# Kernel optimization log

Measured on AMD Instinct MI355X. Metric: run time of the kernel, lower is better.

Reference implementation:

```python
import math
import jax, jax.numpy as jnp
import numpy as np

B, T, D, DFF, E, K = 2, 4096, 1024, 2048, 8, 2
CAP_FACTOR = 1.25


def setup_inputs() -> dict:
    key = jax.random.key(0)
    ks = jax.random.split(key, 5)
    x = jax.random.normal(ks[0], (B, T, D), dtype=jnp.float32)
    gate_w = jax.random.normal(ks[1], (E, D), dtype=jnp.float32) * 0.02
    W1 = jax.random.normal(ks[2], (E, D, DFF), dtype=jnp.float32) * 0.02
    b1 = jnp.zeros((E, DFF), dtype=jnp.float32)
    W2 = jax.random.normal(ks[3], (E, DFF, D), dtype=jnp.float32) * 0.02
    b2 = jnp.zeros((E, D), dtype=jnp.float32)
    return {"x": x, "gate_w": gate_w, "W1": W1, "b1": b1, "W2": W2, "b2": b2}


def _moe_forward(x, gate_w, W1, b1, W2, b2):
    Bs, Ts, Ds = x.shape
    N = Bs * Ts
    x_flat = x.reshape(N, Ds)

    # --- router ---
    logits = x_flat @ gate_w.T                          # (N, E)
    probs = jax.nn.softmax(logits, axis=-1)             # (N, E)
    top_w, top_i = jax.lax.top_k(probs, K)              # (N, K)
    disp_w = top_w / (jnp.sum(top_w, axis=-1, keepdims=True) + 1e-9)

    # --- capacity: slot-major, token-order priority (matches the Python loops) ---
    capacity = max(1, int(math.ceil(CAP_FACTOR * N * K / E)))
    idx_flat = top_i.T.reshape(-1)                       # (K*N,) slot-major order
    oh = jax.nn.one_hot(idx_flat, E, dtype=jnp.int32)    # (K*N, E)
    # position of each assignment within its expert's arrival order
    pos = jnp.sum(jnp.cumsum(oh, axis=0) * oh, axis=-1) - 1  # (K*N,)
    keep = (pos < capacity).reshape(K, N).T              # (N, K)
    w_capped = disp_w * keep.astype(disp_w.dtype)        # (N, K)

    # --- combine weights per expert ---
    oh_nke = jax.nn.one_hot(top_i, E, dtype=w_capped.dtype)   # (N, K, E)
    comb = jnp.einsum('nk,nke->ne', w_capped, oh_nke)         # (N, E)

    # --- experts: dense per-expert FFN, zero-weight tokens contribute nothing ---
    out = jnp.zeros_like(x_flat)
    for e in range(E):
        h = jax.nn.gelu(x_flat @ W1[e] + b1[e], approximate=False)  # (N, DFF)
        y = h @ W2[e] + b2[e]                                        # (N, D)
        out = out + comb[:, e:e + 1] * y

    # --- Switch-style aux load-balancing loss ---
    assigned = (jnp.sum(oh_nke, axis=1) > 0).astype(probs.dtype)  # (N, E)
    f = jnp.mean(assigned, axis=0)
    p = jnp.mean(probs, axis=0)
    aux_loss = E * jnp.sum(f * p)

    return out.reshape(Bs, Ts, Ds), aux_loss


def reference(x, gate_w, W1, b1, W2, b2):
    return _moe_forward(x, gate_w, W1, b1, W2, b2)
```

## Files before the change

kernel.cpp:

```cpp
#include <hip/hip_runtime.h>
#include <hip/hip_bf16.h>
#include <math.h>

#define NB   2
#define NT   4096
#define ND   1024
#define NDFF 2048
#define NE   8
#define NK   2
#define NN   (NB * NT)
#define NCAP 2560

typedef unsigned short ushort_t;
typedef __attribute__((ext_vector_type(8))) short bf16x8;
typedef __attribute__((ext_vector_type(8))) unsigned short u16x8;
typedef __attribute__((ext_vector_type(4))) float f32x4;

__device__ __forceinline__ float gelu_exact(float v) {
  return 0.5f * v * (1.0f + erff(v * 0.70710678118654752f));
}

__device__ __forceinline__ unsigned short f2bf(float f) {
  unsigned int u = __float_as_uint(f);
  u += 0x7fffu + ((u >> 16) & 1u);
  return (unsigned short)(u >> 16);
}
__device__ __forceinline__ float bf2f(unsigned short h) {
  return __uint_as_float(((unsigned int)h) << 16);
}

__device__ __forceinline__ void gl_lds16(const void* g, void* l) {
  __builtin_amdgcn_global_load_lds(
      (__attribute__((address_space(1))) void*)g,
      (__attribute__((address_space(3))) void*)l, 16, 0, 0);
}

__global__ __launch_bounds__(256) void router_kernel(
    const float* __restrict__ x, const float* __restrict__ gw,
    int* __restrict__ top_i, float* __restrict__ disp_w,
    float* __restrict__ p_sum, int* __restrict__ f_cnt) {
  __shared__ float s_p[NE];
  __shared__ int s_f[NE];
  if (threadIdx.x < NE) { s_p[threadIdx.x] = 0.0f; s_f[threadIdx.x] = 0; }
  __syncthreads();

  const int lane = threadIdx.x & 63;
  const int wv = threadIdx.x >> 6;
  const int n = blockIdx.x * 4 + wv;

  const float4* xr = (const float4*)(x + (size_t)n * ND);
  float acc[NE];
#pragma unroll
  for (int e = 0; e < NE; ++e) acc[e] = 0.0f;

#pragma unroll
  for (int q = 0; q < 4; ++q) {
    float4 xv = xr[lane * 4 + q];
#pragma unroll
    for (int e = 0; e < NE; ++e) {
      float4 g = ((const float4*)(gw + (size_t)e * ND))[lane * 4 + q];
      acc[e] += xv.x * g.x + xv.y * g.y + xv.z * g.z + xv.w * g.w;
    }
  }
#pragma unroll
  for (int m = 1; m < 64; m <<= 1) {
#pragma unroll
    for (int e = 0; e < NE; ++e) acc[e] += __shfl_xor(acc[e], m, 64);
  }

  float mx = acc[0];
#pragma unroll
  for (int e = 1; e < NE; ++e) mx = fmaxf(mx, acc[e]);
  float p[NE];
  float s = 0.0f;
#pragma unroll
  for (int e = 0; e < NE; ++e) { p[e] = expf(acc[e] - mx); s += p[e]; }
  float inv = 1.0f / s;
#pragma unroll
  for (int e = 0; e < NE; ++e) p[e] *= inv;

  int i1 = 0; float v1 = p[0];
#pragma unroll
  for (int e = 1; e < NE; ++e) { if (p[e] > v1) { v1 = p[e]; i1 = e; } }
  int i2 = 0; float v2 = -1.0f;
#pragma unroll
  for (int e = 0; e < NE; ++e) { if (e != i1 && p[e] > v2) { v2 = p[e]; i2 = e; } }

  if (lane == 0) {
    float dsum = v1 + v2 + 1e-9f;
    top_i[n * NK + 0] = i1;
    top_i[n * NK + 1] = i2;
    disp_w[n * NK + 0] = v1 / dsum;
    disp_w[n * NK + 1] = v2 / dsum;
#pragma unroll
    for (int e = 0; e < NE; ++e) atomicAdd(&s_p[e], p[e]);
    atomicAdd(&s_f[i1], 1);
    atomicAdd(&s_f[i2], 1);
  }
  __syncthreads();
  if (threadIdx.x < NE) {
    atomicAdd(&p_sum[threadIdx.x], s_p[threadIdx.x]);
    atomicAdd(&f_cnt[threadIdx.x], s_f[threadIdx.x]);
  }
}

__global__ __launch_bounds__(512) void scan_kernel(
    const int* __restrict__ top_i, const float* __restrict__ disp_w,
    int* __restrict__ routed_tok, float* __restrict__ routed_w,
    int* __restrict__ counts, const float* __restrict__ p_sum,
    const int* __restrict__ f_cnt, float* __restrict__ aux_out) {
  __shared__ __align__(16) int s_top[NN * NK];
  for (int i = threadIdx.x; i < (NN * NK) / 4; i += 512)
    ((int4*)s_top)[i] = ((const int4*)top_i)[i];
  __syncthreads();

  const int e = threadIdx.x >> 6;
  const int lane = threadIdx.x & 63;
  int cnt = 0;
  for (int c = 0; c < (NN * NK) / 64; ++c) {
    int a = c * 64 + lane;
    int n = a & (NN - 1);
    int k = a >> 13;
    bool m = (s_top[n * NK + k] == e);
    unsigned long long mask = __ballot(m);
    if (m) {
      int pos = cnt + __popcll(mask & ((1ull << lane) - 1ull));
      if (pos < NCAP) {
        routed_tok[e * NCAP + pos] = n;
        routed_w[e * NCAP + pos] = disp_w[n * NK + k];
      }
    }
    cnt += (int)__popcll(mask);
  }
  if (lane == 0) counts[e] = (cnt < NCAP) ? cnt : NCAP;

  if (threadIdx.x == 0) {
    float aux = 0.0f;
    for (int j = 0; j < NE; ++j)
      aux += (p_sum[j] / (float)NN) * ((float)f_cnt[j] / (float)NN);
    aux_out[0] = aux * (float)NE;
  }
}

__global__ __launch_bounds__(256) void tsplit_kernel(
    const float* __restrict__ W, ushort_t* __restrict__ Thi,
    ushort_t* __restrict__ Tlo, int K, int N) {
  __shared__ float tile[32][33];
  const int t = threadIdx.x;
  const int n0 = blockIdx.x * 32, k0 = blockIdx.y * 32;
  const int r = t >> 3, c4 = (t & 7) * 4;
  float4 v = *(const float4*)(W + (size_t)blockIdx.z * K * N +
                              (size_t)(k0 + r) * N + n0 + c4);
  tile[r][c4 + 0] = v.x; tile[r][c4 + 1] = v.y;
  tile[r][c4 + 2] = v.z; tile[r][c4 + 3] = v.w;
  __syncthreads();
  const int n = t >> 3, kc = (t & 7) * 4;
  ushort4 h, l;
  float f;
  f = tile[kc + 0][n]; h.x = f2bf(f); l.x = f2bf(f - bf2f(h.x));
  f = tile[kc + 1][n]; h.y = f2bf(f); l.y = f2bf(f - bf2f(h.y));
  f = tile[kc + 2][n]; h.z = f2bf(f); l.z = f2bf(f - bf2f(h.z));
  f = tile[kc + 3][n]; h.w = f2bf(f); l.w = f2bf(f - bf2f(h.w));
  size_t o = (size_t)blockIdx.z * N * K + (size_t)(n0 + n) * K + k0 + kc;
  *(ushort4*)(Thi + o) = h;
  *(ushort4*)(Tlo + o) = l;
}

__global__ __launch_bounds__(512, 2) void fgemm_fused(
    const float* __restrict__ x,
    const ushort_t* __restrict__ w1hi, const ushort_t* __restrict__ w1lo,
    const float* __restrict__ b1,
    const ushort_t* __restrict__ w2hi, const ushort_t* __restrict__ w2lo,
    const float* __restrict__ b2,
    const ushort_t* __restrict__ Hrhi, const ushort_t* __restrict__ Hrlo,
    ushort_t* __restrict__ Hwhi, ushort_t* __restrict__ Hwlo,
    const int* __restrict__ routed_tok, const float* __restrict__ routed_w,
    const int* __restrict__ counts, float* __restrict__ outf,
    int n_g1_z, int g1_lo, int g2_lo, int Rh) {
  const int bz = blockIdx.z;
  const bool isG1 = bz < n_g1_z;
  const int e = isG1 ? bz : bz - n_g1_z;
  const int count = counts[e];
  const int chunk_lo = isG1 ? g1_lo : g2_lo;
  const int local0 = blockIdx.y * 128;
  const int row0 = chunk_lo + local0;
  if (row0 >= count) return;
  const int bx = blockIdx.x;
  const int col0 = isG1 ? bx * 256 : (bx & 3) * 256;
  const int koff = isG1 ? 0 : (bx >> 2) * 1024;
  const int Ntot = isG1 ? NDFF : ND;
  const int Bstride = isG1 ? ND : NDFF;

  __shared__ __align__(16) char lds[49152];
  char* ldsA = lds;
  char* ldsB = lds + 16384;

  const int t = threadIdx.x;
  const int lane = t & 63;
  const int wid = t >> 6;
  const int wr = wid >> 2, wc = wid & 3;
  const int fr = lane & 15, ko = lane >> 4;

  const float* srcAf = nullptr;
  char* dstH_ = nullptr; char* dstL_ = nullptr;
  const ushort_t* srcA[2];
  if (isG1) {
    const int r = t >> 2, kc = t & 3;
    const int rr = row0 + r;
    const int tok = routed_tok[e * NCAP + (rr < count ? rr : 0)];
    srcAf = x + (size_t)tok * ND + kc * 8;
    dstH_ = ldsA + (size_t)(r * 8 + (kc ^ (r & 7))) * 16;
    dstL_ = ldsA + (size_t)(r * 8 + ((kc + 4) ^ (r & 7))) * 16;
  } else {
#pragma unroll
    for (int c = 0; c < 2; ++c) {
      int ci = t + 512 * c;
      int r = ci >> 3, bp = ci & 7;
      int bs = bp ^ (r & 7);
      size_t arow = (size_t)e * Rh + local0 + r;
      srcA[c] = (bs < 4 ? Hrhi : Hrlo) + arow * (size_t)NDFF + koff + (bs & 3) * 8;
    }
  }
  const ushort_t* Bh = isG1 ? w1hi : w2hi;
  const ushort_t* Bl = isG1 ? w1lo : w2lo;
  const ushort_t* srcB[4];
#pragma unroll
  for (int c = 0; c < 4; ++c) {
    int ci = t + 512 * c;
    int cc = ci >> 3, bp = ci & 7;
    int bs = bp ^ (cc & 7);
    srcB[c] = (bs < 4 ? Bh : Bl) +
              ((size_t)e * Ntot + col0 + cc) * (size_t)Bstride + koff + (bs & 3) * 8;
  }

  f32x4 acc[4][4] = {};

  for (int ks = 0; ks < 1024; ks += 32) {
    if (isG1) {
      float4 v0 = *(const float4*)(srcAf);
      float4 v1 = *(const float4*)(srcAf + 4);
      srcAf += 32;
      u16x8 hh, ll;
      unsigned short h; float f;
      f = v0.x; h = f2bf(f); hh[0] = h; ll[0] = f2bf(f - bf2f(h));
      f = v0.y; h = f2bf(f); hh[1] = h; ll[1] = f2bf(f - bf2f(h));
      f = v0.z; h = f2bf(f); hh[2] = h; ll[2] = f2bf(f - bf2f(h));
      f = v0.w; h = f2bf(f); hh[3] = h; ll[3] = f2bf(f - bf2f(h));
      f = v1.x; h = f2bf(f); hh[4] = h; ll[4] = f2bf(f - bf2f(h));
      f = v1.y; h = f2bf(f); hh[5] = h; ll[5] = f2bf(f - bf2f(h));
      f = v1.z; h = f2bf(f); hh[6] = h; ll[6] = f2bf(f - bf2f(h));
      f = v1.w; h = f2bf(f); hh[7] = h; ll[7] = f2bf(f - bf2f(h));
      *(u16x8*)dstH_ = hh;
      *(u16x8*)dstL_ = ll;
    } else {
#pragma unroll
      for (int c = 0; c < 2; ++c) {
        gl_lds16(srcA[c], ldsA + (c * 512 + wid * 64) * 16);
        srcA[c] += 32;
      }
    }
#pragma unroll
    for (int c = 0; c < 4; ++c) {
      gl_lds16(srcB[c], ldsB + (c * 512 + wid * 64) * 16);
      srcB[c] += 32;
    }
    __syncthreads();

    bf16x8 Ah[4], Al[4], Bhf[4], Blf[4];
#pragma unroll
    for (int fi = 0; fi < 4; ++fi) {
      int r = wr * 64 + fi * 16 + fr;
      Ah[fi] = *(const bf16x8*)(ldsA + r * 128 + ((ko ^ (r & 7)) << 4));
      Al[fi] = *(const bf16x8*)(ldsA + r * 128 + (((4 + ko) ^ (r & 7)) << 4));
    }
#pragma unroll
    for (int fj = 0; fj < 4; ++fj) {
      int cc = wc * 64 + fj * 16 + fr;
      Bhf[fj] = *(const bf16x8*)(ldsB + cc * 128 + ((ko ^ (cc & 7)) << 4));
      Blf[fj] = *(const bf16x8*)(ldsB + cc * 128 + (((4 + ko) ^ (cc & 7)) << 4));
    }
#pragma unroll
    for (int fi = 0; fi < 4; ++fi)
#pragma unroll
      for (int fj = 0; fj < 4; ++fj) {
        acc[fi][fj] = __builtin_amdgcn_mfma_f32_16x16x32_bf16(
            Ah[fi], Bhf[fj], acc[fi][fj], 0, 0, 0);
        acc[fi][fj] = __builtin_amdgcn_mfma_f32_16x16x32_bf16(
            Ah[fi], Blf[fj], acc[fi][fj], 0, 0, 0);
        acc[fi][fj] = __builtin_amdgcn_mfma_f32_16x16x32_bf16(
            Al[fi], Bhf[fj], acc[fi][fj], 0, 0, 0);
      }
    __syncthreads();
  }

  const float* bias = isG1 ? b1 : b2;
  float bv[4];
#pragma unroll
  for (int fj = 0; fj < 4; ++fj)
    bv[fj] = (koff == 0)
                 ? bias[(size_t)e * Ntot + col0 + wc * 64 + fj * 16 + fr]
                 : 0.0f;

  if (isG1) {
#pragma unroll
    for (int fi = 0; fi < 4; ++fi) {
#pragma unroll
      for (int rg = 0; rg < 4; ++rg) {
        int rr = row0 + wr * 64 + fi * 16 + ko * 4 + rg;
        if (rr < count) {
          size_t rb = ((size_t)e * Rh + (rr - chunk_lo)) * (size_t)NDFF;
#pragma unroll
          for (int fj = 0; fj < 4; ++fj) {
            int cc = col0 + wc * 64 + fj * 16 + fr;
            float g = gelu_exact(acc[fi][fj][rg] + bv[fj]);
            unsigned short hh = f2bf(g);
            Hwhi[rb + cc] = hh;
            Hwlo[rb + cc] = f2bf(g - bf2f(hh));
          }
        }
      }
    }
  } else {
#pragma unroll
    for (int fi = 0; fi < 4; ++fi) {
#pragma unroll
      for (int rg = 0; rg < 4; ++rg) {
        int rr = row0 + wr * 64 + fi * 16 + ko * 4 + rg;
        if (rr < count) {
          int tok = routed_tok[e * NCAP + rr];
          float wgt = routed_w[e * NCAP + rr];
          float* orow = outf + (size_t)tok * ND;
#pragma unroll
          for (int fj = 0; fj < 4; ++fj) {
            int cc = col0 + wc * 64 + fj * 16 + fr;
            atomicAdd(orow + cc, wgt * (acc[fi][fj][rg] + bv[fj]));
          }
        }
      }
    }
  }
}

__global__ __launch_bounds__(256) void gemm1_kernel(
    const float* __restrict__ x, const float* __restrict__ W1,
    const float* __restrict__ b1, const int* __restrict__ routed_tok,
    const int* __restrict__ counts, float* __restrict__ H,
    int e0, size_t h_stride) {
  const int e = e0 + blockIdx.z;
  const int count = counts[e];
  const int row0 = blockIdx.y * 128;
  if (row0 >= count) return;
  const int col0 = blockIdx.x * 128;
  const float* W = W1 + (size_t)e * ND * NDFF;
  float* Hb = H + (size_t)blockIdx.z * h_stride;

  __shared__ __align__(16) float As[16][128];
  __shared__ __align__(16) float Bs[16][128];

  const int tid = threadIdx.x;
  const int arow = tid >> 1;
  const int aq = (tid & 1) * 8;
  const int r = row0 + arow;
  const int tok = routed_tok[e * NCAP + (r < count ? r : 0)];
  const float* Arow = x + (size_t)tok * ND;
  const int bk = tid >> 5;
  const int bc = (tid & 31) * 4;
  const int ty = tid >> 4, tx = tid & 15;

  float c[8][8] = {};

  for (int k0 = 0; k0 < ND; k0 += 16) {
    float4 av0 = *(const float4*)(Arow + k0 + aq);
    float4 av1 = *(const float4*)(Arow + k0 + aq + 4);
    float4 bv0 = *(const float4*)(W + (size_t)(k0 + bk) * NDFF + col0 + bc);
    float4 bv1 = *(const float4*)(W + (size_t)(k0 + bk + 8) * NDFF + col0 + bc);
    __syncthreads();
    As[aq + 0][arow] = av0.x; As[aq + 1][arow] = av0.y;
    As[aq + 2][arow] = av0.z; As[aq + 3][arow] = av0.w;
    As[aq + 4][arow] = av1.x; As[aq + 5][arow] = av1.y;
    As[aq + 6][arow] = av1.z; As[aq + 7][arow] = av1.w;
    *(float4*)&Bs[bk][bc] = bv0;
    *(float4*)&Bs[bk + 8][bc] = bv1;
    __syncthreads();
#pragma unroll
    for (int kk = 0; kk < 16; ++kk) {
      float4 a0 = *(const float4*)&As[kk][ty * 4];
      float4 a1 = *(const float4*)&As[kk][ty * 4 + 64];
      float4 b0 = *(const float4*)&Bs[kk][tx * 4];
      float4 b1r = *(const float4*)&Bs[kk][tx * 4 + 64];
      float ar[8] = {a0.x, a0.y, a0.z, a0.w, a1.x, a1.y, a1.z, a1.w};
      float br[8] = {b0.x, b0.y, b0.z, b0.w, b1r.x, b1r.y, b1r.z, b1r.w};
#pragma unroll
      for (int i = 0; i < 8; ++i)
#pragma unroll
        for (int j = 0; j < 8; ++j)
          c[i][j] = fmaf(ar[i], br[j], c[i][j]);
    }
  }

  const float* b1e = b1 + (size_t)e * NDFF + col0;
#pragma unroll
  for (int i = 0; i < 8; ++i) {
    int rr = row0 + ty * 4 + (i & 3) + (i >> 2) * 64;
    if (rr < count) {
      float* Hr = Hb + (size_t)rr * NDFF + col0;
      float4 v0, v1;
      v0.x = gelu_exact(c[i][0] + b1e[tx * 4 + 0]);
      v0.y = gelu_exact(c[i][1] + b1e[tx * 4 + 1]);
      v0.z = gelu_exact(c[i][2] + b1e[tx * 4 + 2]);
      v0.w = gelu_exact(c[i][3] + b1e[tx * 4 + 3]);
      v1.x = gelu_exact(c[i][4] + b1e[tx * 4 + 64]);
      v1.y = gelu_exact(c[i][5] + b1e[tx * 4 + 65]);
      v1.z = gelu_exact(c[i][6] + b1e[tx * 4 + 66]);
      v1.w = gelu_exact(c[i][7] + b1e[tx * 4 + 67]);
      *(float4*)(Hr + tx * 4) = v0;
      *(float4*)(Hr + tx * 4 + 64) = v1;
    }
  }
}

__global__ __launch_bounds__(256) void gemm2_kernel(
    const float* __restrict__ H, const float* __restrict__ W2,
    const float* __restrict__ b2, const int* __restrict__ routed_tok,
    const float* __restrict__ routed_w, const int* __restrict__ counts,
    float* __restrict__ out, int e0, size_t h_stride) {
  const int e = e0 + blockIdx.z;
  const int count = counts[e];
  const int row0 = blockIdx.y * 128;
  if (row0 >= count) return;
  const int col0 = blockIdx.x * 128;
  const float* W = W2 + (size_t)e * NDFF * ND;
  const float* Hb = H + (size_t)blockIdx.z * h_stride;

  __shared__ __align__(16) float As[16][128];
  __shared__ __align__(16) float Bs[16][128];

  const int tid = threadIdx.x;
  const int arow = tid >> 1;
  const int aq = (tid & 1) * 8;
  const float* Arow = Hb + (size_t)(row0 + arow) * NDFF;
  const int bk = tid >> 5;
  const int bc = (tid & 31) * 4;
  const int ty = tid >> 4, tx = tid & 15;

  float c[8][8] = {};

  for (int k0 = 0; k0 < NDFF; k0 += 16) {
    float4 av0 = *(const float4*)(Arow + k0 + aq);
    float4 av1 = *(const float4*)(Arow + k0 + aq + 4);
    float4 bv0 = *(const float4*)(W + (size_t)(k0 + bk) * ND + col0 + bc);
    float4 bv1 = *(const float4*)(W + (size_t)(k0 + bk + 8) * ND + col0 + bc);
    __syncthreads();
    As[aq + 0][arow] = av0.x; As[aq + 1][arow] = av0.y;
    As[aq + 2][arow] = av0.z; As[aq + 3][arow] = av0.w;
    As[aq + 4][arow] = av1.x; As[aq + 5][arow] = av1.y;
    As[aq + 6][arow] = av1.z; As[aq + 7][arow] = av1.w;
    *(float4*)&Bs[bk][bc] = bv0;
    *(float4*)&Bs[bk + 8][bc] = bv1;
    __syncthreads();
#pragma unroll
    for (int kk = 0; kk < 16; ++kk) {
      float4 a0 = *(const float4*)&As[kk][ty * 4];
      float4 a1 = *(const float4*)&As[kk][ty * 4 + 64];
      float4 b0 = *(const float4*)&Bs[kk][tx * 4];
      float4 b1r = *(const float4*)&Bs[kk][tx * 4 + 64];
      float ar[8] = {a0.x, a0.y, a0.z, a0.w, a1.x, a1.y, a1.z, a1.w};
      float br[8] = {b0.x, b0.y, b0.z, b0.w, b1r.x, b1r.y, b1r.z, b1r.w};
#pragma unroll
      for (int i = 0; i < 8; ++i)
#pragma unroll
        for (int j = 0; j < 8; ++j)
          c[i][j] = fmaf(ar[i], br[j], c[i][j]);
    }
  }

  const float* b2e = b2 + (size_t)e * ND + col0;
#pragma unroll
  for (int i = 0; i < 8; ++i) {
    int rr = row0 + ty * 4 + (i & 3) + (i >> 2) * 64;
    if (rr < count) {
      int tok = routed_tok[e * NCAP + rr];
      float wgt = routed_w[e * NCAP + rr];
      float* orow = out + (size_t)tok * ND + col0;
#pragma unroll
      for (int j = 0; j < 8; ++j) {
        int cc = tx * 4 + (j & 3) + (j >> 2) * 64;
        atomicAdd(orow + cc, wgt * (c[i][j] + b2e[cc]));
      }
    }
  }
}

extern "C" void kernel_launch(void* const* d_in, const int* in_sizes, int n_in,
                              void* d_out, int out_size, void* d_ws, size_t ws_size,
                              hipStream_t stream) {
  const float* x  = (const float*)d_in[0];
  const float* gw = (const float*)d_in[1];
  const float* W1 = (const float*)d_in[2];
  const float* b1 = (const float*)d_in[3];
  const float* W2 = (const float*)d_in[4];
  const float* b2 = (const float*)d_in[5];
  float* out = (float*)d_out;

  char* p = (char*)d_ws;
  auto alloc = [&](size_t bytes) -> char* {
    char* q = p;
    p += (bytes + 255) & ~(size_t)255;
    return q;
  };

  int*   top_i = (int*)alloc((size_t)NN * NK * 4);
  float* dispw = (float*)alloc((size_t)NN * NK * 4);
  int*   rtok  = (int*)alloc((size_t)NE * NCAP * 4);
  float* rw    = (float*)alloc((size_t)NE * NCAP * 4);
  int*   counts = (int*)alloc(256);
  float* psum  = (float*)alloc(64);
  int*   fcnt  = (int*)((char*)psum + 32);
  char*  p_base = p;

  hipMemsetAsync(out, 0, (size_t)NN * ND * 4, stream);
  hipMemsetAsync(psum, 0, 64, stream);

  router_kernel<<<NN / 4, 256, 0, stream>>>(x, gw, top_i, dispw, psum, fcnt);
  scan_kernel<<<1, 512, 0, stream>>>(top_i, dispw, rtok, rw, counts, psum, fcnt,
                                     out + (size_t)NN * ND);

  const size_t sw = (size_t)NE * ND * NDFF * 2;
  const size_t perRow = (size_t)NE * NDFF * 2 * 2;
  size_t wt_end = (size_t)(p_base - (char*)d_ws) + 4 * (sw + 256);
  size_t avail = (ws_size > wt_end + 8192) ? ws_size - wt_end - 8192 : 0;

  int Rh = 0;
  bool full = false;
  if (avail >= (size_t)NCAP * perRow) {
    full = true; Rh = NCAP;
  } else {
    Rh = (int)((avail / (2 * perRow)) & ~(size_t)127);
    if (Rh > NCAP - 128) Rh = NCAP - 128;
  }

  if (Rh >= 128) {
    ushort_t* w1hi = (ushort_t*)alloc(sw);
    ushort_t* w1lo = (ushort_t*)alloc(sw);
    ushort_t* w2hi = (ushort_t*)alloc(sw);
    ushort_t* w2lo = (ushort_t*)alloc(sw);

    tsplit_kernel<<<dim3(NDFF / 32, ND / 32, NE), 256, 0, stream>>>(
        W1, w1hi, w1lo, ND, NDFF);
    tsplit_kernel<<<dim3(ND / 32, NDFF / 32, NE), 256, 0, stream>>>(
        W2, w2hi, w2lo, NDFF, ND);

    const size_t hb = (size_t)NE * Rh * NDFF * 2;
    if (full) {
      ushort_t* Hhi = (ushort_t*)alloc(hb);
      ushort_t* Hlo = (ushort_t*)alloc(hb);
      fgemm_fused<<<dim3(8, NCAP / 128, 8), 512, 0, stream>>>(
          x, w1hi, w1lo, b1, w2hi, w2lo, b2, Hhi, Hlo, Hhi, Hlo,
          rtok, rw, counts, out, 8, 0, 0, Rh);
      fgemm_fused<<<dim3(8, NCAP / 128, 8), 512, 0, stream>>>(
          x, w1hi, w1lo, b1, w2hi, w2lo, b2, Hhi, Hlo, Hhi, Hlo,
          rtok, rw, counts, out, 0, 0, 0, Rh);
    } else {
      ushort_t* h0hi = (ushort_t*)alloc(hb);
      ushort_t* h0lo = (ushort_t*)alloc(hb);
      ushort_t* h1hi = (ushort_t*)alloc(hb);
      ushort_t* h1lo = (ushort_t*)alloc(hb);
      ushort_t* bh[2] = {h0hi, h1hi};
      ushort_t* bl[2] = {h0lo, h1lo};
      const int P = (NCAP + Rh - 1) / Rh;
      const int ylen = Rh / 128;
      fgemm_fused<<<dim3(8, ylen, 8), 512, 0, stream>>>(
          x, w1hi, w1lo, b1, w2hi, w2lo, b2, bh[0], bl[0], bh[0], bl[0],
          rtok, rw, counts, out, 8, 0, 0, Rh);
      for (int i = 1; i < P; ++i) {
        fgemm_fused<<<dim3(8, ylen, 16), 512, 0, stream>>>(
            x, w1hi, w1lo, b1, w2hi, w2lo, b2,
            bh[(i - 1) & 1], bl[(i - 1) & 1], bh[i & 1], bl[i & 1],
            rtok, rw, counts, out, 8, i * Rh, (i - 1) * Rh, Rh);
      }
      fgemm_fused<<<dim3(8, ylen, 8), 512, 0, stream>>>(
          x, w1hi, w1lo, b1, w2hi, w2lo, b2,
          bh[(P - 1) & 1], bl[(P - 1) & 1], bh[(P - 1) & 1], bl[(P - 1) & 1],
          rtok, rw, counts, out, 0, 0, (P - 1) * Rh, Rh);
    }
  } else {
    p = p_base;
    float* H = (float*)p;
    const size_t need_old_full =
        (size_t)(p_base - (char*)d_ws) + (size_t)NE * NCAP * NDFF * 4 + 8192;
    const bool fullH = (ws_size >= need_old_full);
    if (fullH) {
      gemm1_kernel<<<dim3(NDFF / 128, NCAP / 128, NE), 256, 0, stream>>>(
          x, W1, b1, rtok, counts, H, 0, (size_t)NCAP * NDFF);
      gemm2_kernel<<<dim3(ND / 128, NCAP / 128, NE), 256, 0, stream>>>(
          H, W2, b2, rtok, rw, counts, out, 0, (size_t)NCAP * NDFF);
    } else {
      for (int e = 0; e < NE; ++e) {
        gemm1_kernel<<<dim3(NDFF / 128, NCAP / 128, 1), 256, 0, stream>>>(
            x, W1, b1, rtok, counts, H, e, 0);
        gemm2_kernel<<<dim3(ND / 128, NCAP / 128, 1), 256, 0, stream>>>(
            H, W2, b2, rtok, rw, counts, out, e, 0);
      }
    }
  }
}
```

Measured before the change: 1.085 ms.

## Shrink fused GEMM tile to 128x128 with 256 threads, widen weight-split tiles

The fused split-bf16 GEMM goes from 512-thread blocks with 128x256 output tiles to 256-thread blocks with 128x128 tiles. This doubles the grid along x and cuts LDS use per block so that three blocks can sit on a CU. The weight transpose/split kernel moves from 32x32 to 64x64 tiles with wider vector stores. The change trades less operand reuse per tile for more blocks and more occupancy, and each thread now does more loads and conversions per k-step.

```diff
diff --git a/kernel.cpp b/kernel.cpp
--- a/kernel.cpp
+++ b/kernel.cpp
@@ -145,28 +145,45 @@
 __global__ __launch_bounds__(256) void tsplit_kernel(
     const float* __restrict__ W, ushort_t* __restrict__ Thi,
     ushort_t* __restrict__ Tlo, int K, int N) {
-  __shared__ float tile[32][33];
+  __shared__ float tile[64][65];
   const int t = threadIdx.x;
-  const int n0 = blockIdx.x * 32, k0 = blockIdx.y * 32;
-  const int r = t >> 3, c4 = (t & 7) * 4;
-  float4 v = *(const float4*)(W + (size_t)blockIdx.z * K * N +
-                              (size_t)(k0 + r) * N + n0 + c4);
-  tile[r][c4 + 0] = v.x; tile[r][c4 + 1] = v.y;
-  tile[r][c4 + 2] = v.z; tile[r][c4 + 3] = v.w;
+  const int n0 = blockIdx.x * 64, k0 = blockIdx.y * 64;
+  {
+    const int r = t >> 2, c16 = (t & 3) * 16;
+    const float* src = W + (size_t)blockIdx.z * K * N +
+                       (size_t)(k0 + r) * N + n0 + c16;
+#pragma unroll
+    for (int q = 0; q < 4; ++q) {
+      float4 v = *(const float4*)(src + q * 4);
+      tile[r][c16 + q * 4 + 0] = v.x;
+      tile[r][c16 + q * 4 + 1] = v.y;
+      tile[r][c16 + q * 4 + 2] = v.z;
+      tile[r][c16 + q * 4 + 3] = v.w;
+    }
+  }
   __syncthreads();
-  const int n = t >> 3, kc = (t & 7) * 4;
-  ushort4 h, l;
-  float f;
-  f = tile[kc + 0][n]; h.x = f2bf(f); l.x = f2bf(f - bf2f(h.x));
-  f = tile[kc + 1][n]; h.y = f2bf(f); l.y = f2bf(f - bf2f(h.y));
-  f = tile[kc + 2][n]; h.z = f2bf(f); l.z = f2bf(f - bf2f(h.z));
-  f = tile[kc + 3][n]; h.w = f2bf(f); l.w = f2bf(f - bf2f(h.w));
+  const int n = t >> 2, kc = (t & 3) * 16;
+  u16x8 h0, h1, l0, l1;
+#pragma unroll
+  for (int j = 0; j < 8; ++j) {
+    float f = tile[kc + j][n];
+    unsigned short h = f2bf(f);
+    h0[j] = h; l0[j] = f2bf(f - bf2f(h));
+  }
+#pragma unroll
+  for (int j = 0; j < 8; ++j) {
+    float f = tile[kc + 8 + j][n];
+    unsigned short h = f2bf(f);
+    h1[j] = h; l1[j] = f2bf(f - bf2f(h));
+  }
   size_t o = (size_t)blockIdx.z * N * K + (size_t)(n0 + n) * K + k0 + kc;
-  *(ushort4*)(Thi + o) = h;
-  *(ushort4*)(Tlo + o) = l;
-}
-
-__global__ __launch_bounds__(512, 2) void fgemm_fused(
+  *(u16x8*)(Thi + o) = h0;
+  *(u16x8*)(Thi + o + 8) = h1;
+  *(u16x8*)(Tlo + o) = l0;
+  *(u16x8*)(Tlo + o + 8) = l1;
+}
+
+__global__ __launch_bounds__(256, 3) void fgemm_fused(
     const float* __restrict__ x,
     const ushort_t* __restrict__ w1hi, const ushort_t* __restrict__ w1lo,
     const float* __restrict__ b1,
@@ -186,35 +203,38 @@
   const int row0 = chunk_lo + local0;
   if (row0 >= count) return;
   const int bx = blockIdx.x;
-  const int col0 = isG1 ? bx * 256 : (bx & 3) * 256;
-  const int koff = isG1 ? 0 : (bx >> 2) * 1024;
+  const int col0 = isG1 ? bx * 128 : (bx & 7) * 128;
+  const int koff = isG1 ? 0 : (bx >> 3) * 1024;
   const int Ntot = isG1 ? NDFF : ND;
   const int Bstride = isG1 ? ND : NDFF;
 
-  __shared__ __align__(16) char lds[49152];
+  __shared__ __align__(16) char lds[32768];
   char* ldsA = lds;
   char* ldsB = lds + 16384;
 
   const int t = threadIdx.x;
   const int lane = t & 63;
   const int wid = t >> 6;
-  const int wr = wid >> 2, wc = wid & 3;
+  const int wr = wid >> 1, wc = wid & 1;
   const int fr = lane & 15, ko = lane >> 4;
 
   const float* srcAf = nullptr;
-  char* dstH_ = nullptr; char* dstL_ = nullptr;
-  const ushort_t* srcA[2];
+  char* dstA[4] = {nullptr, nullptr, nullptr, nullptr};
+  const ushort_t* srcA[4];
   if (isG1) {
-    const int r = t >> 2, kc = t & 3;
+    const int r = t >> 1, kp = (t & 1) * 2;
     const int rr = row0 + r;
     const int tok = routed_tok[e * NCAP + (rr < count ? rr : 0)];
-    srcAf = x + (size_t)tok * ND + kc * 8;
-    dstH_ = ldsA + (size_t)(r * 8 + (kc ^ (r & 7))) * 16;
-    dstL_ = ldsA + (size_t)(r * 8 + ((kc + 4) ^ (r & 7))) * 16;
+    srcAf = x + (size_t)tok * ND + kp * 8;
+    const int s = r & 7;
+    dstA[0] = ldsA + (size_t)(r * 8 + ((kp + 0) ^ s)) * 16;
+    dstA[1] = ldsA + (size_t)(r * 8 + ((kp + 1) ^ s)) * 16;
+    dstA[2] = ldsA + (size_t)(r * 8 + ((kp + 4) ^ s)) * 16;
+    dstA[3] = ldsA + (size_t)(r * 8 + ((kp + 5) ^ s)) * 16;
   } else {
 #pragma unroll
-    for (int c = 0; c < 2; ++c) {
-      int ci = t + 512 * c;
+    for (int c = 0; c < 4; ++c) {
+      int ci = t + 256 * c;
       int r = ci >> 3, bp = ci & 7;
       int bs = bp ^ (r & 7);
       size_t arow = (size_t)e * Rh + local0 + r;
@@ -226,7 +246,7 @@
   const ushort_t* srcB[4];
 #pragma unroll
   for (int c = 0; c < 4; ++c) {
-    int ci = t + 512 * c;
+    int ci = t + 256 * c;
     int cc = ci >> 3, bp = ci & 7;
     int bs = bp ^ (cc & 7);
     srcB[c] = (bs < 4 ? Bh : Bl) +
@@ -239,29 +259,41 @@
     if (isG1) {
       float4 v0 = *(const float4*)(srcAf);
       float4 v1 = *(const float4*)(srcAf + 4);
+      float4 v2 = *(const float4*)(srcAf + 8);
+      float4 v3 = *(const float4*)(srcAf + 12);
       srcAf += 32;
-      u16x8 hh, ll;
+      u16x8 h0, h1, l0, l1;
       unsigned short h; float f;
-      f = v0.x; h = f2bf(f); hh[0] = h; ll[0] = f2bf(f - bf2f(h));
-      f = v0.y; h = f2bf(f); hh[1] = h; ll[1] = f2bf(f - bf2f(h));
-      f = v0.z; h = f2bf(f); hh[2] = h; ll[2] = f2bf(f - bf2f(h));
-      f = v0.w; h = f2bf(f); hh[3] = h; ll[3] = f2bf(f - bf2f(h));
-      f = v1.x; h = f2bf(f); hh[4] = h; ll[4] = f2bf(f - bf2f(h));
-      f = v1.y; h = f2bf(f); hh[5] = h; ll[5] = f2bf(f - bf2f(h));
-      f = v1.z; h = f2bf(f); hh[6] = h; ll[6] = f2bf(f - bf2f(h));
-      f = v1.w; h = f2bf(f); hh[7] = h; ll[7] = f2bf(f - bf2f(h));
-      *(u16x8*)dstH_ = hh;
-      *(u16x8*)dstL_ = ll;
+      f = v0.x; h = f2bf(f); h0[0] = h; l0[0] = f2bf(f - bf2f(h));
+      f = v0.y; h = f2bf(f); h0[1] = h; l0[1] = f2bf(f - bf2f(h));
+      f = v0.z; h = f2bf(f); h0[2] = h; l0[2] = f2bf(f - bf2f(h));
+      f = v0.w; h = f2bf(f); h0[3] = h; l0[3] = f2bf(f - bf2f(h));
+      f = v1.x; h = f2bf(f); h0[4] = h; l0[4] = f2bf(f - bf2f(h));
+      f = v1.y; h = f2bf(f); h0[5] = h; l0[5] = f2bf(f - bf2f(h));
+      f = v1.z; h = f2bf(f); h0[6] = h; l0[6] = f2bf(f - bf2f(h));
+      f = v1.w; h = f2bf(f); h0[7] = h; l0[7] = f2bf(f - bf2f(h));
+      f = v2.x; h = f2bf(f); h1[0] = h; l1[0] = f2bf(f - bf2f(h));
+      f = v2.y; h = f2bf(f); h1[1] = h; l1[1] = f2bf(f - bf2f(h));
+      f = v2.z; h = f2bf(f); h1[2] = h; l1[2] = f2bf(f - bf2f(h));
+      f = v2.w; h = f2bf(f); h1[3] = h; l1[3] = f2bf(f - bf2f(h));
+      f = v3.x; h = f2bf(f); h1[4] = h; l1[4] = f2bf(f - bf2f(h));
+      f = v3.y; h = f2bf(f); h1[5] = h; l1[5] = f2bf(f - bf2f(h));
+      f = v3.z; h = f2bf(f); h1[6] = h; l1[6] = f2bf(f - bf2f(h));
+      f = v3.w; h = f2bf(f); h1[7] = h; l1[7] = f2bf(f - bf2f(h));
+      *(u16x8*)dstA[0] = h0;
+      *(u16x8*)dstA[1] = h1;
+      *(u16x8*)dstA[2] = l0;
+      *(u16x8*)dstA[3] = l1;
     } else {
 #pragma unroll
-      for (int c = 0; c < 2; ++c) {
-        gl_lds16(srcA[c], ldsA + (c * 512 + wid * 64) * 16);
+      for (int c = 0; c < 4; ++c) {
+        gl_lds16(srcA[c], ldsA + (c * 256 + wid * 64) * 16);
         srcA[c] += 32;
       }
     }
 #pragma unroll
     for (int c = 0; c < 4; ++c) {
-      gl_lds16(srcB[c], ldsB + (c * 512 + wid * 64) * 16);
+      gl_lds16(srcB[c], ldsB + (c * 256 + wid * 64) * 16);
       srcB[c] += 32;
     }
     __syncthreads();
@@ -545,19 +577,19 @@
     ushort_t* w2hi = (ushort_t*)alloc(sw);
     ushort_t* w2lo = (ushort_t*)alloc(sw);
 
-    tsplit_kernel<<<dim3(NDFF / 32, ND / 32, NE), 256, 0, stream>>>(
+    tsplit_kernel<<<dim3(NDFF / 64, ND / 64, NE), 256, 0, stream>>>(
         W1, w1hi, w1lo, ND, NDFF);
-    tsplit_kernel<<<dim3(ND / 32, NDFF / 32, NE), 256, 0, stream>>>(
+    tsplit_kernel<<<dim3(ND / 64, NDFF / 64, NE), 256, 0, stream>>>(
         W2, w2hi, w2lo, NDFF, ND);
 
     const size_t hb = (size_t)NE * Rh * NDFF * 2;
     if (full) {
       ushort_t* Hhi = (ushort_t*)alloc(hb);
       ushort_t* Hlo = (ushort_t*)alloc(hb);
-      fgemm_fused<<<dim3(8, NCAP / 128, 8), 512, 0, stream>>>(
+      fgemm_fused<<<dim3(16, NCAP / 128, 8), 256, 0, stream>>>(
           x, w1hi, w1lo, b1, w2hi, w2lo, b2, Hhi, Hlo, Hhi, Hlo,
           rtok, rw, counts, out, 8, 0, 0, Rh);
-      fgemm_fused<<<dim3(8, NCAP / 128, 8), 512, 0, stream>>>(
+      fgemm_fused<<<dim3(16, NCAP / 128, 8), 256, 0, stream>>>(
           x, w1hi, w1lo, b1, w2hi, w2lo, b2, Hhi, Hlo, Hhi, Hlo,
           rtok, rw, counts, out, 0, 0, 0, Rh);
     } else {
@@ -569,16 +601,16 @@
       ushort_t* bl[2] = {h0lo, h1lo};
       const int P = (NCAP + Rh - 1) / Rh;
       const int ylen = Rh / 128;
-      fgemm_fused<<<dim3(8, ylen, 8), 512, 0, stream>>>(
+      fgemm_fused<<<dim3(16, ylen, 8), 256, 0, stream>>>(
           x, w1hi, w1lo, b1, w2hi, w2lo, b2, bh[0], bl[0], bh[0], bl[0],
           rtok, rw, counts, out, 8, 0, 0, Rh);
       for (int i = 1; i < P; ++i) {
-        fgemm_fused<<<dim3(8, ylen, 16), 512, 0, stream>>>(
+        fgemm_fused<<<dim3(16, ylen, 16), 256, 0, stream>>>(
             x, w1hi, w1lo, b1, w2hi, w2lo, b2,
             bh[(i - 1) & 1], bl[(i - 1) & 1], bh[i & 1], bl[i & 1],
             rtok, rw, counts, out, 8, i * Rh, (i - 1) * Rh, Rh);
       }
-      fgemm_fused<<<dim3(8, ylen, 8), 512, 0, stream>>>(
+      fgemm_fused<<<dim3(16, ylen, 8), 256, 0, stream>>>(
           x, w1hi, w1lo, b1, w2hi, w2lo, b2,
           bh[(P - 1) & 1], bl[(P - 1) & 1], bh[(P - 1) & 1], bl[(P - 1) & 1],
           rtok, rw, counts, out, 0, 0, (P - 1) * Rh, Rh);
```

After: 967.1 us. 1.12x faster.
